# Optimization experiments

Hardware: AMD Instinct MI355X
Metric: run time of the kernel (lower is better)

The kernel has to match this reference:

```python
import jax, jax.numpy as jnp
import numpy as np


def setup_inputs() -> dict:
    key = jax.random.key(0)
    k1, k2, k3 = jax.random.split(key, 3)
    B, E, L, D = 32, 256, 2048, 256
    doc_state = jax.random.normal(k1, (B, L, D), dtype=jnp.float32)
    entity_mapping = jax.random.uniform(k2, (B, E, L), dtype=jnp.float32)
    entity_lens = jax.random.uniform(k3, (B, E), dtype=jnp.float32)
    return {"doc_state": doc_state, "entity_mapping": entity_mapping, "entity_lens": entity_lens}


def reference(doc_state, entity_mapping, entity_lens):
    # Original: (entity_mapping[:, :, :, None] * doc_state[:, None, :, :]).sum(2) / entity_lens[:, :, None]
    # This is a batched contraction over L; express as einsum to avoid the
    # huge [B, E, L, D] intermediate.
    summed = jnp.einsum('bel,bld->bed', entity_mapping, doc_state)  # [B, E, D]
    return summed / entity_lens[:, :, None]
```

## Files before the change

kernel.cpp:

```cpp
#include <hip/hip_runtime.h>
#include <stdint.h>

#define B_ 32
#define E_ 256
#define L_ 2048
#define D_ 256

#define BE 128
#define BD 256
#define BK 32
#define KS 4
#define KCHUNK (L_ / KS)
#define NKT (KCHUNK / BK)

typedef __attribute__((ext_vector_type(2))) float  f32x2;
typedef __attribute__((ext_vector_type(4))) float  f32x4;
typedef __attribute__((ext_vector_type(4))) short  s16x4;
typedef __attribute__((ext_vector_type(8))) short  s16x8;

#define KEYA(row) ((((row) >> 1) & 3) | (((row) & 1) << 2))
#define KEYB(row) (((row) >> 1) & 7)

__device__ __forceinline__ void cvt_hilo1(float x, short &h, short &l) {
    unsigned u = __builtin_bit_cast(unsigned, x);
    h = (short)(u >> 16);
    float hf = __builtin_bit_cast(float, u & 0xFFFF0000u);
    unsigned r = __builtin_bit_cast(unsigned, x - hf);
    l = (short)(r >> 16);
}

__global__ void zero_out_kernel(f32x4* __restrict__ out) {
    out[(size_t)blockIdx.x * 256 + threadIdx.x] = f32x4{0.f, 0.f, 0.f, 0.f};
}

#define LOADT(PA, PB, K0)                                                      \
    {                                                                          \
        _Pragma("unroll")                                                      \
        for (int rr = 0; rr < 2; ++rr)                                         \
            PA[rr] = *(const f32x4*)(Ag + (size_t)(a_r + rr * 64) * L_ + (K0) + a_c4 * 4); \
        _Pragma("unroll")                                                      \
        for (int j = 0; j < 8; ++j)                                            \
            PB[j] = *(const f32x2*)(Sg + (size_t)((K0) + kb * 8 + j) * D_ + dp * 2); \
    }

#define STAGE_CONV(AbN, BbN, PA, PB)                                           \
    {                                                                          \
        _Pragma("unroll")                                                      \
        for (int rr = 0; rr < 2; ++rr) {                                       \
            s16x4 h, l;                                                        \
            _Pragma("unroll")                                                  \
            for (int i = 0; i < 4; ++i) { short hh, ll; cvt_hilo1(PA[rr][i], hh, ll); h[i] = hh; l[i] = ll; } \
            *(s16x4*)&(AbN)[awo_h[rr]] = h;                                    \
            *(s16x4*)&(AbN)[awo_l[rr]] = l;                                    \
        }                                                                      \
        _Pragma("unroll")                                                      \
        for (int dd = 0; dd < 2; ++dd) {                                       \
            s16x8 h, l;                                                        \
            _Pragma("unroll")                                                  \
            for (int j = 0; j < 8; ++j) { short hh, ll; cvt_hilo1(PB[j][dd], hh, ll); h[j] = hh; l[j] = ll; } \
            *(s16x8*)&(BbN)[bwo_h[dd]] = h;                                    \
            *(s16x8*)&(BbN)[bwo_l[dd]] = l;                                    \
        }                                                                      \
    }

#define LGKM_BARRIER()                                                         \
    {                                                                          \
        asm volatile("s_waitcnt lgkmcnt(0)" ::: "memory");                     \
        __builtin_amdgcn_s_barrier();                                          \
        asm volatile("" ::: "memory");                                         \
    }

#define ITER(K, AbC, BbC, AbN, BbN, PA, PB)                                    \
    {                                                                          \
        s16x8 bh[4], bl[4], ah[4], al[4];                                      \
        _Pragma("unroll")                                                      \
        for (int ni = 0; ni < 4; ++ni) {                                       \
            bh[ni] = *(const s16x8*)&(BbC)[bro_h[ni]];                         \
            bl[ni] = *(const s16x8*)&(BbC)[bro_l[ni]];                         \
        }                                                                      \
        _Pragma("unroll")                                                      \
        for (int mi = 0; mi < 4; ++mi) {                                       \
            ah[mi] = *(const s16x8*)&(AbC)[aro_h[mi]];                         \
            al[mi] = *(const s16x8*)&(AbC)[aro_l[mi]];                         \
        }                                                                      \
        if ((K) + 1 < NKT) {                                                   \
            STAGE_CONV(AbN, BbN, PA, PB)                                       \
            if ((K) + 3 < NKT) LOADT(PA, PB, ((K) + 3) * BK)                   \
        }                                                                      \
        __builtin_amdgcn_s_setprio(1);                                         \
        _Pragma("unroll")                                                      \
        for (int mi = 0; mi < 4; ++mi)                                         \
            _Pragma("unroll")                                                  \
            for (int ni = 0; ni < 4; ++ni) {                                   \
                acc[mi][ni] = __builtin_amdgcn_mfma_f32_16x16x32_bf16(ah[mi], bh[ni], acc[mi][ni], 0, 0, 0); \
                acc[mi][ni] = __builtin_amdgcn_mfma_f32_16x16x32_bf16(ah[mi], bl[ni], acc[mi][ni], 0, 0, 0); \
                acc[mi][ni] = __builtin_amdgcn_mfma_f32_16x16x32_bf16(al[mi], bh[ni], acc[mi][ni], 0, 0, 0); \
            }                                                                  \
        __builtin_amdgcn_s_setprio(0);                                         \
        if ((K) + 1 < NKT) LGKM_BARRIER()                                      \
    }

__global__ __launch_bounds__(512, 2)
void mean_pool_kernel(const float* __restrict__ doc,
                      const float* __restrict__ emap,
                      const float* __restrict__ lens,
                      float* __restrict__ out) {
    __shared__ __align__(16) short As[2][BE][64];
    __shared__ __align__(16) short Bs[2][BD][64];
    __shared__ float lens_s[BE];

    const int t   = threadIdx.x;
    const int blk = blockIdx.x;
    const int ks  = blk & 3;
    const int e0  = ((blk >> 2) & 1) * BE;
    const int b   = blk >> 3;

    const float* Ag = emap + ((size_t)b * E_ + e0) * L_ + ks * KCHUNK;
    const float* Sg = doc  + (size_t)b * L_ * D_ + (size_t)ks * KCHUNK * D_;

    if (t < BE) lens_s[t] = lens[b * E_ + e0 + t];

    const int a_c4 = t & 7;
    const int a_r  = t >> 3;
    const int dp   = t & 127;
    const int kb   = t >> 7;

    const int lane = t & 63;
    const int w    = t >> 6;
    const int eo   = (w & 1) * 64;
    const int dq   = (w >> 1) * 64;
    const int ml   = lane & 15;
    const int kg   = lane >> 4;

    int awo_h[2], awo_l[2];
    #pragma unroll
    for (int rr = 0; rr < 2; ++rr) {
        const int row = a_r + rr * 64, k = KEYA(row), hb = (a_c4 & 1) * 4;
        awo_h[rr] = row * 64 + ((((a_c4 >> 1)    ) ^ k) << 3) + hb;
        awo_l[rr] = row * 64 + ((((a_c4 >> 1) | 4) ^ k) << 3) + hb;
    }
    int bwo_h[2], bwo_l[2];
    #pragma unroll
    for (int dd = 0; dd < 2; ++dd) {
        const int row = dp * 2 + dd, k = KEYB(row);
        bwo_h[dd] = row * 64 + (((kb    ) ^ k) << 3);
        bwo_l[dd] = row * 64 + (((kb | 4) ^ k) << 3);
    }
    int aro_h[4], aro_l[4], bro_h[4], bro_l[4];
    #pragma unroll
    for (int i = 0; i < 4; ++i) {
        const int ar = eo + i * 16 + ml, ka = KEYA(ar);
        aro_h[i] = ar * 64 + (((kg    ) ^ ka) << 3);
        aro_l[i] = ar * 64 + (((kg | 4) ^ ka) << 3);
        const int br = dq + i * 16 + ml, kB = KEYB(br);
        bro_h[i] = br * 64 + (((kg    ) ^ kB) << 3);
        bro_l[i] = br * 64 + (((kg | 4) ^ kB) << 3);
    }

    f32x4 acc[4][4] = {};
    f32x4 paE[2], paO[2];
    f32x2 pbE[8], pbO[8];

    LOADT(paE, pbE, 0)
    LOADT(paO, pbO, BK)
    STAGE_CONV(&As[0][0][0], &Bs[0][0][0], paE, pbE)
    LOADT(paE, pbE, 2 * BK)
    LGKM_BARRIER()

    for (int kt = 0; kt < NKT; kt += 2) {
        ITER(kt,     (&As[0][0][0]), (&Bs[0][0][0]), (&As[1][0][0]), (&Bs[1][0][0]), paO, pbO)
        ITER(kt + 1, (&As[1][0][0]), (&Bs[1][0][0]), (&As[0][0][0]), (&Bs[0][0][0]), paE, pbE)
    }

    #pragma unroll
    for (int mi = 0; mi < 4; ++mi) {
        #pragma unroll
        for (int rr = 0; rr < 4; ++rr) {
            const int er = eo + mi * 16 + kg * 4 + rr;
            const float lv = lens_s[er];
            #pragma unroll
            for (int ni = 0; ni < 4; ++ni)
                atomicAdd(&out[((size_t)(b * E_ + e0 + er)) * D_ + dq + ni * 16 + ml],
                          acc[mi][ni][rr] / lv);
        }
    }
}

extern "C" void kernel_launch(void* const* d_in, const int* in_sizes, int n_in,
                              void* d_out, int out_size, void* d_ws, size_t ws_size,
                              hipStream_t stream) {
    const float* doc  = (const float*)d_in[0];
    const float* emap = (const float*)d_in[1];
    const float* lens = (const float*)d_in[2];
    float* out = (float*)d_out;

    zero_out_kernel<<<dim3(out_size / (4 * 256)), dim3(256), 0, stream>>>((f32x4*)out);

    dim3 grid(B_ * (E_ / BE) * (D_ / BD) * KS);
    dim3 block(512);
    hipLaunchKernelGGL(mean_pool_kernel, grid, block, 0, stream,
                       doc, emap, lens, out);
}
```

Baseline: 176.8 us.

## Stage entity_mapping in 128-wide LDS super-chunks and remap block indices

The A operand (entity_mapping) is now loaded in wide 128-column super-chunks. Each row gets a 512-byte contiguous fetch, which is split into hi/lo bf16 halves and written to a single-buffered LDS region, with one barrier per super-chunk instead of per-tile A staging. The B tile pipeline is kept, and only B is converted inside each ITER. Block indices are also remapped so that neighbouring blocks pair batches differently, which may change cache locality. The cost is a larger LDS footprint and 32 more live registers of prefetched A across iterations, which may reduce occupancy or cause spills.

```diff
diff --git a/kernel.cpp b/kernel.cpp
--- a/kernel.cpp
+++ b/kernel.cpp
@@ -12,13 +12,13 @@
 #define KS 4
 #define KCHUNK (L_ / KS)
 #define NKT (KCHUNK / BK)
+#define SUP 128
 
 typedef __attribute__((ext_vector_type(2))) float  f32x2;
 typedef __attribute__((ext_vector_type(4))) float  f32x4;
 typedef __attribute__((ext_vector_type(4))) short  s16x4;
 typedef __attribute__((ext_vector_type(8))) short  s16x8;
 
-#define KEYA(row) ((((row) >> 1) & 3) | (((row) & 1) << 2))
 #define KEYB(row) (((row) >> 1) & 7)
 
 __device__ __forceinline__ void cvt_hilo1(float x, short &h, short &l) {
@@ -33,26 +33,34 @@
     out[(size_t)blockIdx.x * 256 + threadIdx.x] = f32x4{0.f, 0.f, 0.f, 0.f};
 }
 
-#define LOADT(PA, PB, K0)                                                      \
-    {                                                                          \
-        _Pragma("unroll")                                                      \
-        for (int rr = 0; rr < 2; ++rr)                                         \
-            PA[rr] = *(const f32x4*)(Ag + (size_t)(a_r + rr * 64) * L_ + (K0) + a_c4 * 4); \
+#define LOAD_A(RA, SS)                                                         \
+    {                                                                          \
+        _Pragma("unroll")                                                      \
+        for (int rr = 0; rr < 8; ++rr)                                         \
+            RA[rr] = *(const f32x4*)(Ag + (size_t)(rr * 16 + a_sr) * L_ + (SS) * SUP + a_sc * 4); \
+    }
+
+#define WRITE_A(RA)                                                            \
+    {                                                                          \
+        _Pragma("unroll")                                                      \
+        for (int rr = 0; rr < 8; ++rr) {                                       \
+            s16x4 h, l;                                                        \
+            _Pragma("unroll")                                                  \
+            for (int i = 0; i < 4; ++i) { short hh, ll; cvt_hilo1(RA[rr][i], hh, ll); h[i] = hh; l[i] = ll; } \
+            *(s16x4*)&A_hi[awoff + rr * 2048] = h;                             \
+            *(s16x4*)&A_lo[awoff + rr * 2048] = l;                             \
+        }                                                                      \
+    }
+
+#define LOADT_B(PB, K0)                                                        \
+    {                                                                          \
         _Pragma("unroll")                                                      \
         for (int j = 0; j < 8; ++j)                                            \
             PB[j] = *(const f32x2*)(Sg + (size_t)((K0) + kb * 8 + j) * D_ + dp * 2); \
     }
 
-#define STAGE_CONV(AbN, BbN, PA, PB)                                           \
-    {                                                                          \
-        _Pragma("unroll")                                                      \
-        for (int rr = 0; rr < 2; ++rr) {                                       \
-            s16x4 h, l;                                                        \
-            _Pragma("unroll")                                                  \
-            for (int i = 0; i < 4; ++i) { short hh, ll; cvt_hilo1(PA[rr][i], hh, ll); h[i] = hh; l[i] = ll; } \
-            *(s16x4*)&(AbN)[awo_h[rr]] = h;                                    \
-            *(s16x4*)&(AbN)[awo_l[rr]] = l;                                    \
-        }                                                                      \
+#define STAGE_B(BbN, PB)                                                       \
+    {                                                                          \
         _Pragma("unroll")                                                      \
         for (int dd = 0; dd < 2; ++dd) {                                       \
             s16x8 h, l;                                                        \
@@ -70,7 +78,7 @@
         asm volatile("" ::: "memory");                                         \
     }
 
-#define ITER(K, AbC, BbC, AbN, BbN, PA, PB)                                    \
+#define ITER(K, S, BbC, BbN, PB)                                               \
     {                                                                          \
         s16x8 bh[4], bl[4], ah[4], al[4];                                      \
         _Pragma("unroll")                                                      \
@@ -80,12 +88,13 @@
         }                                                                      \
         _Pragma("unroll")                                                      \
         for (int mi = 0; mi < 4; ++mi) {                                       \
-            ah[mi] = *(const s16x8*)&(AbC)[aro_h[mi]];                         \
-            al[mi] = *(const s16x8*)&(AbC)[aro_l[mi]];                         \
+            const int aoff = abase[mi] + ((((S) * 4 + kg) ^ akey[mi]) << 3);   \
+            ah[mi] = *(const s16x8*)&A_hi[aoff];                               \
+            al[mi] = *(const s16x8*)&A_lo[aoff];                               \
         }                                                                      \
         if ((K) + 1 < NKT) {                                                   \
-            STAGE_CONV(AbN, BbN, PA, PB)                                       \
-            if ((K) + 3 < NKT) LOADT(PA, PB, ((K) + 3) * BK)                   \
+            STAGE_B(BbN, PB)                                                   \
+            if ((K) + 3 < NKT) LOADT_B(PB, ((K) + 3) * BK)                     \
         }                                                                      \
         __builtin_amdgcn_s_setprio(1);                                         \
         _Pragma("unroll")                                                      \
@@ -105,40 +114,39 @@
                       const float* __restrict__ emap,
                       const float* __restrict__ lens,
                       float* __restrict__ out) {
-    __shared__ __align__(16) short As[2][BE][64];
+    __shared__ __align__(16) short A_hi[BE * SUP];
+    __shared__ __align__(16) short A_lo[BE * SUP];
     __shared__ __align__(16) short Bs[2][BD][64];
     __shared__ float lens_s[BE];
 
-    const int t   = threadIdx.x;
-    const int blk = blockIdx.x;
-    const int ks  = blk & 3;
-    const int e0  = ((blk >> 2) & 1) * BE;
-    const int b   = blk >> 3;
+    const int t  = threadIdx.x;
+    const int bi = blockIdx.x;
+    const int r   = bi & 7;
+    const int q   = bi >> 3;
+    const int ks  = r & 3;
+    const int b   = (q >> 1) * 2 + (r >> 2);
+    const int e0  = (q & 1) * BE;
 
     const float* Ag = emap + ((size_t)b * E_ + e0) * L_ + ks * KCHUNK;
     const float* Sg = doc  + (size_t)b * L_ * D_ + (size_t)ks * KCHUNK * D_;
 
     if (t < BE) lens_s[t] = lens[b * E_ + e0 + t];
 
-    const int a_c4 = t & 7;
-    const int a_r  = t >> 3;
-    const int dp   = t & 127;
-    const int kb   = t >> 7;
+    const int a_sr = t >> 5;
+    const int a_sc = t & 31;
+    const int akey_w = a_sr & 7;
+    const int awoff = a_sr * SUP + (((a_sc >> 1) ^ akey_w) << 3) + (a_sc & 1) * 4;
+
+    const int dp = t & 127;
+    const int kb = t >> 7;
 
     const int lane = t & 63;
     const int w    = t >> 6;
     const int eo   = (w & 1) * 64;
-    const int dq   = (w >> 1) * 64;
+    const int dq   = (w >> 1) * 32 * 2;
     const int ml   = lane & 15;
     const int kg   = lane >> 4;
 
-    int awo_h[2], awo_l[2];
-    #pragma unroll
-    for (int rr = 0; rr < 2; ++rr) {
-        const int row = a_r + rr * 64, k = KEYA(row), hb = (a_c4 & 1) * 4;
-        awo_h[rr] = row * 64 + ((((a_c4 >> 1)    ) ^ k) << 3) + hb;
-        awo_l[rr] = row * 64 + ((((a_c4 >> 1) | 4) ^ k) << 3) + hb;
-    }
     int bwo_h[2], bwo_l[2];
     #pragma unroll
     for (int dd = 0; dd < 2; ++dd) {
@@ -146,30 +154,37 @@
         bwo_h[dd] = row * 64 + (((kb    ) ^ k) << 3);
         bwo_l[dd] = row * 64 + (((kb | 4) ^ k) << 3);
     }
-    int aro_h[4], aro_l[4], bro_h[4], bro_l[4];
+    int abase[4], akey[4], bro_h[4], bro_l[4];
     #pragma unroll
     for (int i = 0; i < 4; ++i) {
-        const int ar = eo + i * 16 + ml, ka = KEYA(ar);
-        aro_h[i] = ar * 64 + (((kg    ) ^ ka) << 3);
-        aro_l[i] = ar * 64 + (((kg | 4) ^ ka) << 3);
+        const int ar = eo + i * 16 + ml;
+        abase[i] = ar * SUP;
+        akey[i]  = ar & 7;
         const int br = dq + i * 16 + ml, kB = KEYB(br);
         bro_h[i] = br * 64 + (((kg    ) ^ kB) << 3);
         bro_l[i] = br * 64 + (((kg | 4) ^ kB) << 3);
     }
 
     f32x4 acc[4][4] = {};
-    f32x4 paE[2], paO[2];
+    f32x4 ra[8];
     f32x2 pbE[8], pbO[8];
 
-    LOADT(paE, pbE, 0)
-    LOADT(paO, pbO, BK)
-    STAGE_CONV(&As[0][0][0], &Bs[0][0][0], paE, pbE)
-    LOADT(paE, pbE, 2 * BK)
-    LGKM_BARRIER()
-
-    for (int kt = 0; kt < NKT; kt += 2) {
-        ITER(kt,     (&As[0][0][0]), (&Bs[0][0][0]), (&As[1][0][0]), (&Bs[1][0][0]), paO, pbO)
-        ITER(kt + 1, (&As[1][0][0]), (&Bs[1][0][0]), (&As[0][0][0]), (&Bs[0][0][0]), paE, pbE)
+    LOAD_A(ra, 0)
+    LOADT_B(pbE, 0)
+    LOADT_B(pbO, BK)
+    STAGE_B((&Bs[0][0][0]), pbE)
+    LOADT_B(pbE, 2 * BK)
+
+    for (int ss = 0; ss < 4; ++ss) {
+        WRITE_A(ra)
+        if (ss < 3) LOAD_A(ra, ss + 1)
+        LGKM_BARRIER()
+
+        const int kt = ss * 4;
+        ITER(kt + 0, 0, (&Bs[0][0][0]), (&Bs[1][0][0]), pbO)
+        ITER(kt + 1, 1, (&Bs[1][0][0]), (&Bs[0][0][0]), pbE)
+        ITER(kt + 2, 2, (&Bs[0][0][0]), (&Bs[1][0][0]), pbO)
+        ITER(kt + 3, 3, (&Bs[1][0][0]), (&Bs[0][0][0]), pbE)
     }
 
     #pragma unroll
```

New measurement: 180.3 us. 2.0% more time.
